# Performance work log

Measured on AMD Instinct MI355X. Metric: run time of the kernel, lower is better.

The kernel has to match this reference:

```python
import jax, jax.numpy as jnp
import numpy as np


def setup_inputs() -> dict:
    key = jax.random.key(0)
    k0, k1, k2, k3, k4 = jax.random.split(key, 5)
    n, c, s, h, w = 4, 128, 31, 32, 22
    x = jax.random.normal(k0, (n, c, s, h, w), dtype=jnp.float32)
    # 1x1 conv to a single channel == per-pixel dot over channels + scalar bias
    scale = 1.0 / np.sqrt(c).astype(np.float32)
    w1 = jax.random.normal(k1, (c,), dtype=jnp.float32) * scale
    b1 = jax.random.normal(k2, (), dtype=jnp.float32) * 0.01
    w2 = jax.random.normal(k3, (c,), dtype=jnp.float32) * scale
    b2 = jax.random.normal(k4, (), dtype=jnp.float32) * 0.01
    return {"x": x, "w1": w1, "b1": b1, "w2": w2, "b2": b2, "top_k": 16}


def reference(x, w1, b1, w2, b2, top_k):
    n, c, s, h, w = x.shape
    hw = h * w
    ns = n * (s - 1)
    # adjacent-frame pairs; 1x1 conv (C->1) as channel contraction
    X0 = jnp.einsum('ncshw,c->nshw', x[:, :, : s - 1], w1) + b1  # (n, s-1, h, w)
    X1 = jnp.einsum('ncshw,c->nshw', x[:, :, 1:], w2) + b2       # (n, s-1, h, w)
    X0 = X0.reshape(ns, hw)
    X1 = X1.reshape(ns, hw)
    # outer-product scores per frame pair, softmax over last dim
    attention = jax.nn.softmax(X0[:, :, None] * X1[:, None, :], axis=2)  # (ns, hw, hw)
    # top-k values along last dim -> (ns, hw, k); torch .view(ns, k, h, w)
    # is a raw row-major reinterpretation, so a plain reshape is faithful.
    vals, _ = jax.lax.top_k(attention, top_k)
    vals = vals.reshape(n, s - 1, top_k, h, w)
    # trans_out: (n, s-1, k, h, w) -> (n, k, s-1, h, w)
    return jnp.transpose(vals, (0, 2, 1, 3, 4))
```

## Files before the change

### kernel.cpp

```cpp
#include <hip/hip_runtime.h>
#include <math.h>

#define NB   4
#define C    128
#define S    31
#define HW   704
#define T    30
#define NS   120
#define K    16

__global__ __launch_bounds__(256) void conv_kernel(
    const float* __restrict__ x,
    const float* __restrict__ w1, const float* __restrict__ b1p,
    const float* __restrict__ w2, const float* __restrict__ b2p,
    float* __restrict__ A, float* __restrict__ B) {
  const int tid  = threadIdx.x;
  const int lane = tid & 63;
  const int cg   = tid >> 6;
  const int g    = blockIdx.x * 64 + lane;
  const int fr   = g / 176;
  const int f4   = g % 176;
  const int sf   = fr % S;
  const int n    = fr / S;

  const float4* xp =
      (const float4*)(x + (((size_t)(n * C + cg * 32) * S + sf) * HW)) + f4;
  float4 a1 = make_float4(0.f, 0.f, 0.f, 0.f);
  float4 a2 = make_float4(0.f, 0.f, 0.f, 0.f);
#pragma unroll
  for (int c = 0; c < 32; ++c) {
    float4 xv = xp[(size_t)c * (S * HW / 4)];
    const float wa = w1[cg * 32 + c];
    const float wb = w2[cg * 32 + c];
    a1.x = fmaf(xv.x, wa, a1.x); a1.y = fmaf(xv.y, wa, a1.y);
    a1.z = fmaf(xv.z, wa, a1.z); a1.w = fmaf(xv.w, wa, a1.w);
    a2.x = fmaf(xv.x, wb, a2.x); a2.y = fmaf(xv.y, wb, a2.y);
    a2.z = fmaf(xv.z, wb, a2.z); a2.w = fmaf(xv.w, wb, a2.w);
  }
  __shared__ float4 s1[4][64];
  __shared__ float4 s2[4][64];
  s1[cg][lane] = a1;
  s2[cg][lane] = a2;
  __syncthreads();
  if (tid < 64) {
    float4 r1 = s1[0][tid], r2 = s2[0][tid];
#pragma unroll
    for (int u = 1; u < 4; ++u) {
      float4 t1 = s1[u][tid], t2 = s2[u][tid];
      r1.x += t1.x; r1.y += t1.y; r1.z += t1.z; r1.w += t1.w;
      r2.x += t2.x; r2.y += t2.y; r2.z += t2.z; r2.w += t2.w;
    }
    const float bb1 = b1p[0], bb2 = b2p[0];
    r1.x += bb1; r1.y += bb1; r1.z += bb1; r1.w += bb1;
    r2.x += bb2; r2.y += bb2; r2.z += bb2; r2.w += bb2;
    if (sf < T)
      ((float4*)(A + (size_t)(n * T + sf) * HW))[f4] = r1;
    if (sf >= 1)
      ((float4*)(B + (size_t)(n * T + sf - 1) * HW))[f4] = r2;
  }
}

__global__ __launch_bounds__(256) void softmax_select_kernel(
    const float* __restrict__ A, const float* __restrict__ B,
    float* __restrict__ out) {
  __shared__ float4 bs4[176];
  __shared__ float  partial[4][64];
  __shared__ float  seltop[K], selbot[K];
  const int tid  = threadIdx.x;
  const int lane = tid & 63;
  const int w    = tid >> 6;
  const int i    = blockIdx.x / 11;
  const int slab = blockIdx.x % 11;
  const int n    = i / T;
  const int tp   = i % T;

  if (tid < 176) bs4[tid] = ((const float4*)(B + i * HW))[tid];
  const int   r = slab * 64 + lane;
  const float a = A[i * HW + r];
  __syncthreads();

  if (tid < 64) {
    const float* bs = (const float*)&bs4[0];
    float vt[11], vb[11];
#pragma unroll
    for (int j = 0; j < 11; ++j) {
      const float v = bs[j * 64 + tid];
      vt[j] = v;
      vb[j] = v;
    }
#pragma unroll 1
    for (int rr = 0; rr < K; ++rr) {
      float lmT = vt[0], lmB = vb[0];
#pragma unroll
      for (int j = 1; j < 11; ++j) {
        lmT = fmaxf(lmT, vt[j]);
        lmB = fminf(lmB, vb[j]);
      }
      float gT = lmT, gB = lmB;
#pragma unroll
      for (int off = 1; off < 64; off <<= 1) {
        gT = fmaxf(gT, __shfl_xor(gT, off, 64));
        gB = fminf(gB, __shfl_xor(gB, off, 64));
      }
      const unsigned long long mT = __ballot(lmT == gT);
      const unsigned long long mB = __ballot(lmB == gB);
      if (tid == (int)(__ffsll(mT) - 1)) {
        bool done = false;
#pragma unroll
        for (int j = 0; j < 11; ++j) {
          const bool hit = (!done) && (vt[j] == gT);
          vt[j] = hit ? -INFINITY : vt[j];
          done  = done || hit;
        }
      }
      if (tid == (int)(__ffsll(mB) - 1)) {
        bool done = false;
#pragma unroll
        for (int j = 0; j < 11; ++j) {
          const bool hit = (!done) && (vb[j] == gB);
          vb[j] = hit ? INFINITY : vb[j];
          done  = done || hit;
        }
      }
      if (tid == 0) {
        seltop[rr] = gT;
        selbot[rr] = gB;
      }
    }
  }
  __syncthreads();

  const float st0 = seltop[0];
  const float sb0 = selbot[0];
  const float L2E = 1.4426950408889634f;
  const float a2  = a * L2E;
  const float nm  = -((a >= 0.f) ? a * st0 : a * sb0) * L2E;

  float p0 = 0.f, p1 = 0.f, p2 = 0.f, p3 = 0.f;
#pragma unroll 11
  for (int j = 0; j < 44; ++j) {
    const float4 bq = bs4[w * 44 + j];
    p0 += __builtin_amdgcn_exp2f(fmaf(a2, bq.x, nm));
    p1 += __builtin_amdgcn_exp2f(fmaf(a2, bq.y, nm));
    p2 += __builtin_amdgcn_exp2f(fmaf(a2, bq.z, nm));
    p3 += __builtin_amdgcn_exp2f(fmaf(a2, bq.w, nm));
  }
  partial[w][lane] = (p0 + p1) + (p2 + p3);
  __syncthreads();

  if (w == 0) {
    const float part =
        (partial[0][lane] + partial[1][lane]) +
        (partial[2][lane] + partial[3][lane]);
    const float rp = 1.f / part;
    float ov[16];
#pragma unroll
    for (int t = 0; t < K; ++t) {
      const float sel = (a >= 0.f) ? seltop[t] : selbot[t];
      ov[t] = __builtin_amdgcn_exp2f(fmaf(a2, sel, nm)) * rp;
    }
    float* op = out + (((size_t)(n * K + r / 44)) * T + tp) * HW + (r % 44) * K;
#pragma unroll
    for (int t4 = 0; t4 < 4; ++t4)
      ((float4*)op)[t4] = ((const float4*)ov)[t4];
  }
}

extern "C" void kernel_launch(void* const* d_in, const int* in_sizes, int n_in,
                              void* d_out, int out_size, void* d_ws, size_t ws_size,
                              hipStream_t stream) {
  (void)in_sizes; (void)n_in; (void)out_size; (void)ws_size;
  const float* x  = (const float*)d_in[0];
  const float* w1 = (const float*)d_in[1];
  const float* b1 = (const float*)d_in[2];
  const float* w2 = (const float*)d_in[3];
  const float* b2 = (const float*)d_in[4];
  float* out = (float*)d_out;

  float* A = (float*)d_ws;
  float* B = A + NS * HW;

  conv_kernel<<<341, 256, 0, stream>>>(x, w1, b1, w2, b2, A, B);
  softmax_select_kernel<<<NS * 11, 256, 0, stream>>>(A, B, out);
}
```

Measured before the change: 109.5 us.

## Move per-frame top-k selection into conv kernel and merge partial lists

The conv kernel now works per frame in three chunks. Each chunk runs a 16-round wave-level top/bottom selection over its slice of B and writes partial top-16 and bottom-16 lists to workspace. The softmax kernel then merges the three partial lists with bitonic shuffle merges instead of repeating a full 704-element selection in each of the 11 slab blocks per frame. This removes redundant selection work but adds a serial selection tail to the conv kernel and extra workspace traffic.

```diff
diff --git a/kernel.cpp b/kernel.cpp
--- a/kernel.cpp
+++ b/kernel.cpp
@@ -9,22 +9,25 @@
 #define NS   120
 #define K    16
 
-__global__ __launch_bounds__(256) void conv_kernel(
+__global__ __launch_bounds__(256) void conv_select_kernel(
     const float* __restrict__ x,
     const float* __restrict__ w1, const float* __restrict__ b1p,
     const float* __restrict__ w2, const float* __restrict__ b2p,
-    float* __restrict__ A, float* __restrict__ B) {
-  const int tid  = threadIdx.x;
-  const int lane = tid & 63;
-  const int cg   = tid >> 6;
-  const int g    = blockIdx.x * 64 + lane;
-  const int fr   = g / 176;
-  const int f4   = g % 176;
-  const int sf   = fr % S;
-  const int n    = fr / S;
+    float* __restrict__ A, float* __restrict__ B,
+    float* __restrict__ ptop, float* __restrict__ pbot) {
+  const int tid   = threadIdx.x;
+  const int lane  = tid & 63;
+  const int cg    = tid >> 6;
+  const int fr    = blockIdx.x / 3;
+  const int chunk = blockIdx.x % 3;
+  const int sf    = fr % S;
+  const int n     = fr / S;
+  const int f4    = chunk * 64 + lane;
+  const bool act  = f4 < 176;
+  const int f4c   = act ? f4 : 175;
 
   const float4* xp =
-      (const float4*)(x + (((size_t)(n * C + cg * 32) * S + sf) * HW)) + f4;
+      (const float4*)(x + (((size_t)(n * C + cg * 32) * S + sf) * HW)) + f4c;
   float4 a1 = make_float4(0.f, 0.f, 0.f, 0.f);
   float4 a2 = make_float4(0.f, 0.f, 0.f, 0.f);
 #pragma unroll
@@ -53,15 +56,69 @@
     const float bb1 = b1p[0], bb2 = b2p[0];
     r1.x += bb1; r1.y += bb1; r1.z += bb1; r1.w += bb1;
     r2.x += bb2; r2.y += bb2; r2.z += bb2; r2.w += bb2;
-    if (sf < T)
-      ((float4*)(A + (size_t)(n * T + sf) * HW))[f4] = r1;
-    if (sf >= 1)
-      ((float4*)(B + (size_t)(n * T + sf - 1) * HW))[f4] = r2;
+    const bool act2 = (chunk * 64 + tid) < 176;
+    if (act2) {
+      if (sf < T)
+        ((float4*)(A + (size_t)(n * T + sf) * HW))[chunk * 64 + tid] = r1;
+      if (sf >= 1)
+        ((float4*)(B + (size_t)(n * T + sf - 1) * HW))[chunk * 64 + tid] = r2;
+    }
+    s2[0][tid] = r2;
+  }
+  __syncthreads();
+
+  if (tid < 64 && sf >= 1) {
+    const int i = n * T + sf - 1;
+    const int nv = (chunk == 2) ? 3 : 4;
+    const float* bs = (const float*)&s2[0][0];
+    float vt[4], vb[4];
+#pragma unroll
+    for (int j = 0; j < 3; ++j) {
+      const float v = bs[j * 64 + tid];
+      vt[j] = v; vb[j] = v;
+    }
+    if (nv == 4) { const float v = bs[192 + tid]; vt[3] = v; vb[3] = v; }
+    else         { vt[3] = -INFINITY;         vb[3] = INFINITY; }
+    float* pt = ptop + (i * 3 + chunk) * K;
+    float* pb = pbot + (i * 3 + chunk) * K;
+#pragma unroll 1
+    for (int rr = 0; rr < K; ++rr) {
+      float lmT = fmaxf(fmaxf(vt[0], vt[1]), fmaxf(vt[2], vt[3]));
+      float lmB = fminf(fminf(vb[0], vb[1]), fminf(vb[2], vb[3]));
+      float gT = lmT, gB = lmB;
+#pragma unroll
+      for (int off = 1; off < 64; off <<= 1) {
+        gT = fmaxf(gT, __shfl_xor(gT, off, 64));
+        gB = fminf(gB, __shfl_xor(gB, off, 64));
+      }
+      const unsigned long long mT = __ballot(lmT == gT);
+      const unsigned long long mB = __ballot(lmB == gB);
+      if (tid == (int)(__ffsll(mT) - 1)) {
+        bool done = false;
+#pragma unroll
+        for (int j = 0; j < 4; ++j) {
+          const bool hit = (!done) && (vt[j] == gT);
+          vt[j] = hit ? -INFINITY : vt[j];
+          done  = done || hit;
+        }
+      }
+      if (tid == (int)(__ffsll(mB) - 1)) {
+        bool done = false;
+#pragma unroll
+        for (int j = 0; j < 4; ++j) {
+          const bool hit = (!done) && (vb[j] == gB);
+          vb[j] = hit ? INFINITY : vb[j];
+          done  = done || hit;
+        }
+      }
+      if (tid == 0) { pt[rr] = gT; pb[rr] = gB; }
+    }
   }
 }
 
-__global__ __launch_bounds__(256) void softmax_select_kernel(
+__global__ __launch_bounds__(256) void softmax_merge_kernel(
     const float* __restrict__ A, const float* __restrict__ B,
+    const float* __restrict__ ptop, const float* __restrict__ pbot,
     float* __restrict__ out) {
   __shared__ float4 bs4[176];
   __shared__ float  partial[4][64];
@@ -77,56 +134,43 @@
   if (tid < 176) bs4[tid] = ((const float4*)(B + i * HW))[tid];
   const int   r = slab * 64 + lane;
   const float a = A[i * HW + r];
-  __syncthreads();
-
-  if (tid < 64) {
-    const float* bs = (const float*)&bs4[0];
-    float vt[11], vb[11];
-#pragma unroll
-    for (int j = 0; j < 11; ++j) {
-      const float v = bs[j * 64 + tid];
-      vt[j] = v;
-      vb[j] = v;
-    }
-#pragma unroll 1
-    for (int rr = 0; rr < K; ++rr) {
-      float lmT = vt[0], lmB = vb[0];
-#pragma unroll
-      for (int j = 1; j < 11; ++j) {
-        lmT = fmaxf(lmT, vt[j]);
-        lmB = fminf(lmB, vb[j]);
-      }
-      float gT = lmT, gB = lmB;
-#pragma unroll
-      for (int off = 1; off < 64; off <<= 1) {
-        gT = fmaxf(gT, __shfl_xor(gT, off, 64));
-        gB = fminf(gB, __shfl_xor(gB, off, 64));
-      }
-      const unsigned long long mT = __ballot(lmT == gT);
-      const unsigned long long mB = __ballot(lmB == gB);
-      if (tid == (int)(__ffsll(mT) - 1)) {
-        bool done = false;
-#pragma unroll
-        for (int j = 0; j < 11; ++j) {
-          const bool hit = (!done) && (vt[j] == gT);
-          vt[j] = hit ? -INFINITY : vt[j];
-          done  = done || hit;
-        }
-      }
-      if (tid == (int)(__ffsll(mB) - 1)) {
-        bool done = false;
-#pragma unroll
-        for (int j = 0; j < 11; ++j) {
-          const bool hit = (!done) && (vb[j] == gB);
-          vb[j] = hit ? INFINITY : vb[j];
-          done  = done || hit;
-        }
-      }
-      if (tid == 0) {
-        seltop[rr] = gT;
-        selbot[rr] = gB;
-      }
-    }
+
+  if (w == 0) {
+    const float* pt = ptop + i * 3 * K;
+    float e = -INFINITY;
+    if (lane < 16)       e = pt[lane];
+    else if (lane < 32)  e = pt[47 - lane];
+#pragma unroll
+    for (int off = 16; off >= 1; off >>= 1) {
+      const float xx = __shfl_xor(e, off, 64);
+      e = (lane & off) ? fminf(e, xx) : fmaxf(e, xx);
+    }
+    if (lane >= 32)      e = -INFINITY;
+    else if (lane >= 16) e = pt[63 - lane];
+#pragma unroll
+    for (int off = 16; off >= 1; off >>= 1) {
+      const float xx = __shfl_xor(e, off, 64);
+      e = (lane & off) ? fminf(e, xx) : fmaxf(e, xx);
+    }
+    if (lane < 16) seltop[lane] = e;
+  } else if (w == 1) {
+    const float* pb = pbot + i * 3 * K;
+    float e = INFINITY;
+    if (lane < 16)       e = pb[lane];
+    else if (lane < 32)  e = pb[47 - lane];
+#pragma unroll
+    for (int off = 16; off >= 1; off >>= 1) {
+      const float xx = __shfl_xor(e, off, 64);
+      e = (lane & off) ? fmaxf(e, xx) : fminf(e, xx);
+    }
+    if (lane >= 32)      e = INFINITY;
+    else if (lane >= 16) e = pb[63 - lane];
+#pragma unroll
+    for (int off = 16; off >= 1; off >>= 1) {
+      const float xx = __shfl_xor(e, off, 64);
+      e = (lane & off) ? fmaxf(e, xx) : fminf(e, xx);
+    }
+    if (lane < 16) selbot[lane] = e;
   }
   __syncthreads();
 
@@ -177,9 +221,12 @@
   const float* b2 = (const float*)d_in[4];
   float* out = (float*)d_out;
 
-  float* A = (float*)d_ws;
-  float* B = A + NS * HW;
-
-  conv_kernel<<<341, 256, 0, stream>>>(x, w1, b1, w2, b2, A, B);
-  softmax_select_kernel<<<NS * 11, 256, 0, stream>>>(A, B, out);
+  float* A    = (float*)d_ws;
+  float* B    = A + NS * HW;
+  float* ptop = B + NS * HW;
+  float* pbot = ptop + NS * 3 * K;
+
+  conv_select_kernel<<<372, 256, 0, stream>>>(x, w1, b1, w2, b2,
+                                              A, B, ptop, pbot);
+  softmax_merge_kernel<<<NS * 11, 256, 0, stream>>>(A, B, ptop, pbot, out);
 }
```

Result: no change. 107.5 us, median of 2 (-1.9%).
